# Optimization experiments

Measured on AMD Instinct MI355X. Metric: run time of the kernel, lower is better.

Reference implementation:

```python
import jax, jax.numpy as jnp
import numpy as np

B, F, V_IN = 8, 64, 163842  # icosahedron order 7
V_OUT, K = 40962, 7         # order 6, 1-ring (6 neighbors + self)


def setup_inputs() -> dict:
    key = jax.random.key(0)
    kx, ki = jax.random.split(key)
    x = jax.random.normal(kx, (B, F, V_IN), dtype=jnp.float32)
    neigh_indices = jax.random.randint(ki, (V_OUT, K), 0, V_IN, dtype=jnp.int64)
    return {"x": x, "neigh_indices": neigh_indices}


def reference(x, neigh_indices):
    # Gather fixed-size 1-ring neighborhoods: (B, F, V_OUT, K)
    gathered = x[:, :, neigh_indices]
    # Mean pooling over the neighborhood axis (pooling_type='mean')
    pooled = jnp.mean(gathered, axis=-1)  # (B, F, V_OUT)
    # Original returns (pooled, max_pool_indices=None); indices are None for mean.
    return pooled
```

## Files before the change

kernel.cpp:

```cpp
#include <hip/hip_runtime.h>


typedef float    f2 __attribute__((ext_vector_type(2)));
typedef float    f8 __attribute__((ext_vector_type(8)));
typedef _Float16 h8 __attribute__((ext_vector_type(8)));
typedef unsigned int u4 __attribute__((ext_vector_type(4)));

constexpr int B = 8, F = 64, V_IN = 163842, V_OUT = 40962, K = 7;
constexpr int ROWS = B * F;
constexpr int RG   = 8;
constexpr int NG   = ROWS / RG;
constexpr int TPB  = 256;
constexpr int GPX  = NG / 8;
constexpr int CPB1 = 2 * TPB;
constexpr int IBX  = (V_IN + CPB1 - 1) / CPB1;
constexpr int VB   = (V_OUT + TPB - 1) / TPB;
constexpr int BLOCKS2 = 8 * GPX * VB;
constexpr size_t XH_BYTES = (size_t)NG * V_IN * 16;

__global__ __launch_bounds__(TPB) void icopool_pack_h8(
    const float* __restrict__ x, u4* __restrict__ xH)
{
    const int g  = blockIdx.y;
    const int c0 = blockIdx.x * CPB1 + threadIdx.x * 2;
    if (c0 >= V_IN) return;
    const float* xp = x + (size_t)g * RG * V_IN + c0;
    h8 e0, e1;
    #pragma unroll
    for (int r = 0; r < 8; ++r) {
        const f2 v = __builtin_nontemporal_load((const f2*)(xp + (size_t)r * V_IN));
        e0[r] = (_Float16)v.x;
        e1[r] = (_Float16)v.y;
    }
    union { h8 h; u4 u; } cv0, cv1;
    cv0.h = e0; cv1.h = e1;
    u4* dst = xH + ((size_t)g * V_IN + c0);
    dst[0] = cv0.u;
    dst[1] = cv1.u;
}

__global__ __launch_bounds__(TPB) void icopool_gather_h8(
    const u4* __restrict__ xH,
    const int* __restrict__ nidx,
    float*     __restrict__ out)
{
    __shared__ int sidx[TPB * K];
    __shared__ int limiter[8192];
    const int b   = blockIdx.x;
    const int xcd = b & 7;
    const int j   = b >> 3;
    const int gl  = j / VB;
    const int vb  = j % VB;
    const int t   = threadIdx.x;

    const int fbase = vb * (TPB * K);
    #pragma unroll
    for (int k = 0; k < K; ++k) {
        const int off = k * TPB + t;
        sidx[off] = (fbase + off < V_OUT * K) ? nidx[fbase + off] : 0;
    }
    if (t == 0) limiter[0] = 1;
    __syncthreads();

    const int v = vb * TPB + t;
    if (v >= V_OUT) return;
    const int g = xcd * GPX + gl;

    const int* my = sidx + t * K;
    const u4* s = xH + (size_t)g * V_IN;
    const u4 q0 = s[(size_t)my[0]];
    const u4 q1 = s[(size_t)my[1]];
    const u4 q2 = s[(size_t)my[2]];
    const u4 q3 = s[(size_t)my[3]];
    const u4 q4 = s[(size_t)my[4]];
    const u4 q5 = s[(size_t)my[5]];
    const u4 q6 = s[(size_t)my[6]];

    union { u4 u; h8 h; } c0, c1, c2, c3, c4, c5, c6;
    c0.u = q0; c1.u = q1; c2.u = q2; c3.u = q3; c4.u = q4; c5.u = q5; c6.u = q6;
    f8 acc = __builtin_convertvector(c0.h, f8);
    acc += __builtin_convertvector(c1.h, f8);
    acc += __builtin_convertvector(c2.h, f8);
    acc += __builtin_convertvector(c3.h, f8);
    acc += __builtin_convertvector(c4.h, f8);
    acc += __builtin_convertvector(c5.h, f8);
    acc += __builtin_convertvector(c6.h, f8);
    acc *= (1.0f / 7.0f);

    float* o = out + (size_t)(g * RG) * V_OUT + v;
    #pragma unroll
    for (int rr = 0; rr < 8; ++rr)
        __builtin_nontemporal_store(acc[rr], o + (size_t)rr * V_OUT);
}

constexpr int RPB  = 2;
constexpr int RGS  = ROWS / RPB;
constexpr int RG_PER_XCD = RGS / 8;
constexpr int VB1  = (V_OUT + TPB - 1) / TPB;
constexpr int BLOCKS_V1  = RGS * VB1;

__global__ __launch_bounds__(TPB) void icopool_gather(
    const float* __restrict__ x,
    const int*   __restrict__ nidx,
    float*       __restrict__ out)
{
    const int b        = blockIdx.x;
    const int xcd      = b & 7;
    const int j        = b >> 3;
    const int rg_local = j / VB1;
    const int vb       = j % VB1;
    const int rg       = xcd * RG_PER_XCD + rg_local;
    const int r0       = rg * RPB;

    const int v = vb * TPB + threadIdx.x;
    if (v >= V_OUT) return;

    const int base = v * K;
    const int i0 = nidx[base + 0];
    const int i1 = nidx[base + 1];
    const int i2 = nidx[base + 2];
    const int i3 = nidx[base + 3];
    const int i4 = nidx[base + 4];
    const int i5 = nidx[base + 5];
    const int i6 = nidx[base + 6];

    #pragma unroll
    for (int r = 0; r < RPB; ++r) {
        const float* xr = x + (size_t)(r0 + r) * V_IN;
        float sum = xr[i0] + xr[i1] + xr[i2] + xr[i3] + xr[i4] + xr[i5] + xr[i6];
        __builtin_nontemporal_store(sum * (1.0f / 7.0f),
                                    out + (size_t)(r0 + r) * V_OUT + v);
    }
}

extern "C" void kernel_launch(void* const* d_in, const int* in_sizes, int n_in,
                              void* d_out, int out_size, void* d_ws, size_t ws_size,
                              hipStream_t stream) {
    const float* x    = (const float*)d_in[0];
    const int*   nidx = (const int*)d_in[1];
    float*       out  = (float*)d_out;

    if (ws_size >= XH_BYTES && d_ws != nullptr) {
        u4* xH = (u4*)d_ws;
        icopool_pack_h8<<<dim3(IBX, NG), dim3(TPB), 0, stream>>>(x, xH);
        icopool_gather_h8<<<dim3(BLOCKS2), dim3(TPB), 0, stream>>>(xH, nidx, out);
    } else {
        icopool_gather<<<dim3(BLOCKS_V1), dim3(TPB), 0, stream>>>(x, nidx, out);
    }
}
```

Before: 541.0 us.

## Fuse fp16 pack and gather into one kernel with per-group spin barrier

Merges the separate pack and gather kernels into one launch. Each block converts a slice of its row group's input into packed fp16 in the workspace, then signals an atomic counter and spins until all blocks of that group have arrived, and then gathers. Every block of a group runs on the same XCD, so the freshly packed data can still be in that XCD's L2 when it is read, and the second launch and full-grid boundary go away. The barrier assumes all blocks of a group are resident at once; if they are not, it can deadlock. The old shared-memory occupancy limiter is dropped, and a small zeroing kernel is added for the flags.

Result: slower. 820.1 us (+51.6%).

```diff
diff --git a/kernel.cpp b/kernel.cpp
--- a/kernel.cpp
+++ b/kernel.cpp
@@ -1,9 +1,9 @@
 #include <hip/hip_runtime.h>
 
 
-typedef float    f2 __attribute__((ext_vector_type(2)));
-typedef float    f8 __attribute__((ext_vector_type(8)));
-typedef _Float16 h8 __attribute__((ext_vector_type(8)));
+typedef float    f4v __attribute__((ext_vector_type(4)));
+typedef float    f8  __attribute__((ext_vector_type(8)));
+typedef _Float16 h8  __attribute__((ext_vector_type(8)));
 typedef unsigned int u4 __attribute__((ext_vector_type(4)));
 
 constexpr int B = 8, F = 64, V_IN = 163842, V_OUT = 40962, K = 7;
@@ -12,46 +12,74 @@
 constexpr int NG   = ROWS / RG;
 constexpr int TPB  = 256;
 constexpr int GPX  = NG / 8;
-constexpr int CPB1 = 2 * TPB;
-constexpr int IBX  = (V_IN + CPB1 - 1) / CPB1;
 constexpr int VB   = (V_OUT + TPB - 1) / TPB;
-constexpr int BLOCKS2 = 8 * GPX * VB;
-constexpr size_t XH_BYTES = (size_t)NG * V_IN * 16;
+constexpr int CPG  = 1020;
+constexpr int BLOCKS = NG * VB;
+constexpr size_t XH_BYTES  = (size_t)NG * V_IN * 16;
+constexpr size_t FLAGS_OFF = (XH_BYTES + 255) & ~(size_t)255;
+constexpr int FLAG_STRIDE  = 16;
+constexpr size_t WS_NEED   = FLAGS_OFF + (size_t)NG * FLAG_STRIDE * 4;
 
-__global__ __launch_bounds__(TPB) void icopool_pack_h8(
-    const float* __restrict__ x, u4* __restrict__ xH)
+__global__ __launch_bounds__(64) void icopool_zero(int* __restrict__ flags)
 {
-    const int g  = blockIdx.y;
-    const int c0 = blockIdx.x * CPB1 + threadIdx.x * 2;
-    if (c0 >= V_IN) return;
-    const float* xp = x + (size_t)g * RG * V_IN + c0;
-    h8 e0, e1;
-    #pragma unroll
-    for (int r = 0; r < 8; ++r) {
-        const f2 v = __builtin_nontemporal_load((const f2*)(xp + (size_t)r * V_IN));
-        e0[r] = (_Float16)v.x;
-        e1[r] = (_Float16)v.y;
-    }
-    union { h8 h; u4 u; } cv0, cv1;
-    cv0.h = e0; cv1.h = e1;
-    u4* dst = xH + ((size_t)g * V_IN + c0);
-    dst[0] = cv0.u;
-    dst[1] = cv1.u;
+    flags[threadIdx.x * FLAG_STRIDE] = 0;
 }
 
-__global__ __launch_bounds__(TPB) void icopool_gather_h8(
-    const u4* __restrict__ xH,
-    const int* __restrict__ nidx,
-    float*     __restrict__ out)
+__global__ __launch_bounds__(TPB) void icopool_fused(
+    const float* __restrict__ x,
+    u4*          __restrict__ xH,
+    int*         __restrict__ flags,
+    const int*   __restrict__ nidx,
+    float*       __restrict__ out)
 {
     __shared__ int sidx[TPB * K];
-    __shared__ int limiter[8192];
-    const int b   = blockIdx.x;
-    const int xcd = b & 7;
-    const int j   = b >> 3;
+    const int bid = blockIdx.x;
+    const int xcd = bid & 7;
+    const int j   = bid >> 3;
     const int gl  = j / VB;
     const int vb  = j % VB;
+    const int g   = xcd * GPX + gl;
     const int t   = threadIdx.x;
+
+    {
+        const int c0 = vb * CPG + t * 4;
+        const int cend = (vb + 1) * CPG;
+        if (c0 < cend && c0 < V_IN) {
+            const float* xg = x + (size_t)g * RG * V_IN;
+            if (c0 + 3 < V_IN) {
+                h8 e0, e1, e2, e3;
+                #pragma unroll
+                for (int r = 0; r < RG; ++r) {
+                    const f4v vv = __builtin_nontemporal_load(
+                        (const f4v*)(xg + (size_t)r * V_IN + c0));
+                    e0[r] = (_Float16)vv.x;
+                    e1[r] = (_Float16)vv.y;
+                    e2[r] = (_Float16)vv.z;
+                    e3[r] = (_Float16)vv.w;
+                }
+                union { h8 h; u4 u; } u0, u1, u2, u3;
+                u0.h = e0; u1.h = e1; u2.h = e2; u3.h = e3;
+                u4* dst = xH + (size_t)g * V_IN + c0;
+                dst[0] = u0.u;
+                dst[1] = u1.u;
+                dst[2] = u2.u;
+                dst[3] = u3.u;
+            } else {
+                #pragma unroll
+                for (int cc = 0; cc < 4; ++cc) {
+                    const int c = c0 + cc;
+                    if (c < V_IN) {
+                        h8 e;
+                        #pragma unroll
+                        for (int r = 0; r < RG; ++r)
+                            e[r] = (_Float16)xg[(size_t)r * V_IN + c];
+                        union { h8 h; u4 u; } cv; cv.h = e;
+                        xH[(size_t)g * V_IN + c] = cv.u;
+                    }
+                }
+            }
+        }
+    }
 
     const int fbase = vb * (TPB * K);
     #pragma unroll
@@ -59,12 +87,19 @@
         const int off = k * TPB + t;
         sidx[off] = (fbase + off < V_OUT * K) ? nidx[fbase + off] : 0;
     }
-    if (t == 0) limiter[0] = 1;
+
+    asm volatile("s_waitcnt vmcnt(0)" ::: "memory");
+    __syncthreads();
+    if (t == 0) {
+        int* fp = flags + g * FLAG_STRIDE;
+        __hip_atomic_fetch_add(fp, 1, __ATOMIC_RELAXED, __HIP_MEMORY_SCOPE_AGENT);
+        while (__hip_atomic_load(fp, __ATOMIC_RELAXED, __HIP_MEMORY_SCOPE_AGENT) < VB)
+            __builtin_amdgcn_s_sleep(8);
+    }
     __syncthreads();
 
     const int v = vb * TPB + t;
     if (v >= V_OUT) return;
-    const int g = xcd * GPX + gl;
 
     const int* my = sidx + t * K;
     const u4* s = xH + (size_t)g * V_IN;
@@ -140,10 +175,11 @@
     const int*   nidx = (const int*)d_in[1];
     float*       out  = (float*)d_out;
 
-    if (ws_size >= XH_BYTES && d_ws != nullptr) {
-        u4* xH = (u4*)d_ws;
-        icopool_pack_h8<<<dim3(IBX, NG), dim3(TPB), 0, stream>>>(x, xH);
-        icopool_gather_h8<<<dim3(BLOCKS2), dim3(TPB), 0, stream>>>(xH, nidx, out);
+    if (ws_size >= WS_NEED && d_ws != nullptr) {
+        u4*  xH    = (u4*)d_ws;
+        int* flags = (int*)((char*)d_ws + FLAGS_OFF);
+        icopool_zero<<<dim3(1), dim3(64), 0, stream>>>(flags);
+        icopool_fused<<<dim3(BLOCKS), dim3(TPB), 0, stream>>>(x, xH, flags, nidx, out);
     } else {
         icopool_gather<<<dim3(BLOCKS_V1), dim3(TPB), 0, stream>>>(x, nidx, out);
     }
```
